# Kernel optimization log

Measured on AMD Instinct MI355X. Metric: run time of the kernel, lower is better.

## Reference

```python
import jax, jax.numpy as jnp
import numpy as np

N_NODES = 100000
LN_EPS = 1e-5
NEG_SLOPE = 0.2


def setup_inputs() -> dict:
    key = jax.random.key(0)
    ks = jax.random.split(key, 6)
    N, E, NIN, EDIM, NOUT, H = N_NODES, 1600000, 64, 32, 128, 4
    x = jax.random.normal(ks[0], (N, NIN), dtype=jnp.float32)
    edge_index = jax.random.randint(ks[1], (2, E), 0, N, dtype=jnp.int64)
    edge_attr = jax.random.normal(ks[2], (E, EDIM), dtype=jnp.float32)
    # xavier-uniform linear weights (torch layout: [out, in])
    def xavier(k, fan_out, fan_in):
        lim = float(np.sqrt(6.0 / (fan_in + fan_out)))
        return jax.random.uniform(k, (fan_out, fan_in), jnp.float32, -lim, lim)
    W_msg = xavier(ks[3], NOUT, NIN + EDIM)          # (128, 96)
    W_att = xavier(ks[4], H, 2 * NIN + EDIM)         # (4, 160)
    bias = jnp.zeros((NOUT,), jnp.float32)
    ln_gamma = jnp.ones((NOUT,), jnp.float32)
    ln_beta = jnp.zeros((NOUT,), jnp.float32)
    return {"x": x, "edge_index": edge_index, "edge_attr": edge_attr,
            "W_msg": W_msg, "W_att": W_att, "bias": bias,
            "ln_gamma": ln_gamma, "ln_beta": ln_beta}


def reference(x, edge_index, edge_attr, W_msg, W_att, bias, ln_gamma, ln_beta):
    N = x.shape[0]
    H = W_att.shape[0]
    src, dst = edge_index[0], edge_index[1]
    xs = x[src]                                       # (E, node_in) gather
    xd = x[dst]                                       # (E, node_in) gather
    # message: W_msg @ [h_u ; x_uv]
    msg_in = jnp.concatenate([xs, edge_attr], axis=-1)            # (E, 96)
    msgs = msg_in @ W_msg.T                                        # (E, out_dim)
    msgs = msgs.reshape(-1, H, W_msg.shape[0] // H)                # (E, H, D)
    # attention logits: LeakyReLU(W_att @ [h_u ; h_v ; x_uv])
    att_in = jnp.concatenate([xs, xd, edge_attr], axis=-1)         # (E, 160)
    logits = att_in @ W_att.T                                      # (E, H)
    logits = jax.nn.leaky_relu(logits, NEG_SLOPE)
    # per-destination-node sparse softmax
    seg_max = jax.ops.segment_max(logits, dst, num_segments=N)     # (N, H)
    exp_l = jnp.exp(logits - seg_max[dst])                         # (E, H)
    seg_sum = jax.ops.segment_sum(exp_l, dst, num_segments=N)      # (N, H)
    att = exp_l / (seg_sum[dst] + 1e-9)                            # (E, H)
    # weighted scatter-add aggregation
    weighted = msgs * att[..., None]                               # (E, H, D)
    out = jax.ops.segment_sum(weighted, dst, num_segments=N)       # (N, H, D)
    out = out.reshape(N, -1) + bias                                # concat heads
    # layer norm over feature dim
    mu = out.mean(axis=-1, keepdims=True)
    var = out.var(axis=-1, keepdims=True)
    out = (out - mu) * jax.lax.rsqrt(var + LN_EPS) * ln_gamma + ln_beta
    return out
```

## Files before the change

### kernel.cpp

```cpp
#include <hip/hip_runtime.h>
#include <hip/hip_bf16.h>

typedef __attribute__((ext_vector_type(8))) short short8;
typedef __attribute__((ext_vector_type(4))) float f32x4;

__device__ __forceinline__ unsigned short fbf(float f) {
  union { float f; unsigned u; } v; v.f = f;
  unsigned r = v.u + 0x7fffu + ((v.u >> 16) & 1u);
  return (unsigned short)(r >> 16);
}
__device__ __forceinline__ unsigned pk2(float a, float b) {
  return (unsigned)fbf(a) | ((unsigned)fbf(b) << 16);
}
__device__ __forceinline__ float ubf(unsigned hi) {
  union { unsigned u; float f; } v; v.u = hi << 16; return v.f;
}
__device__ __forceinline__ float ubf_lo(unsigned u) {
  union { unsigned u; float f; } v; v.u = u << 16; return v.f;
}
__device__ __forceinline__ float ubf_hi(unsigned u) {
  union { unsigned u; float f; } v; v.u = u & 0xffff0000u; return v.f;
}
__device__ __forceinline__ float dot4(float4 a, float4 b) {
  return fmaf(a.x, b.x, fmaf(a.y, b.y, fmaf(a.z, b.z, a.w * b.w)));
}

__launch_bounds__(256)
__global__ void k_phase1(const float* __restrict__ x, const float* __restrict__ W_att,
                         const int* __restrict__ edst, int E,
                         float4* __restrict__ A_s, float4* __restrict__ A_d,
                         unsigned* __restrict__ xb32, int* __restrict__ deg,
                         int* __restrict__ rank, int N) {
  __shared__ float4 s_wa[160];
  if (threadIdx.x < 160) s_wa[threadIdx.x] = ((const float4*)W_att)[threadIdx.x];
  for (int i = blockIdx.x * blockDim.x + threadIdx.x; i < E; i += gridDim.x * blockDim.x)
    rank[i] = atomicAdd(&deg[edst[i]], 1);
  __syncthreads();
  for (int v = blockIdx.x * blockDim.x + threadIdx.x; v < N; v += gridDim.x * blockDim.x) {
    const float4* xp = (const float4*)&x[v * 64];
    float4 xq[16];
    #pragma unroll
    for (int k = 0; k < 16; k++) xq[k] = xp[k];
    float as[4] = {}, ad[4] = {};
    #pragma unroll
    for (int h = 0; h < 4; h++) {
      #pragma unroll
      for (int k = 0; k < 16; k++) {
        as[h] += dot4(s_wa[h * 40 + k], xq[k]);
        ad[h] += dot4(s_wa[h * 40 + 16 + k], xq[k]);
      }
    }
    A_s[v] = make_float4(as[0], as[1], as[2], as[3]);
    A_d[v] = make_float4(ad[0], ad[1], ad[2], ad[3]);
    #pragma unroll
    for (int k = 0; k < 16; k++) {
      xb32[v * 32 + 2 * k]     = pk2(xq[k].x, xq[k].y);
      xb32[v * 32 + 2 * k + 1] = pk2(xq[k].z, xq[k].w);
    }
  }
}

__global__ void k_scan1(const int* __restrict__ deg, int N, int* __restrict__ part,
                        int* __restrict__ bsum) {
  __shared__ int tmp[1024];
  int tid = threadIdx.x;
  int i = blockIdx.x * 1024 + tid;
  int dv = (i < N) ? deg[i] : 0;
  int v = (dv + 7) & ~7;
  tmp[tid] = v;
  __syncthreads();
  for (int ofs = 1; ofs < 1024; ofs <<= 1) {
    int t = (tid >= ofs) ? tmp[tid - ofs] : 0;
    __syncthreads();
    tmp[tid] += t;
    __syncthreads();
  }
  if (i < N) part[i] = tmp[tid] - v;
  if (tid == 1023) bsum[blockIdx.x] = tmp[tid];
}

__global__ void k_scan2(int* __restrict__ part, const int* __restrict__ bsum,
                        const int* __restrict__ deg, int N, int4* __restrict__ csrp) {
  __shared__ int sbase;
  if (threadIdx.x == 0) {
    int b = 0;
    for (int j = 0; j < (int)blockIdx.x; j++) b += bsum[j];
    sbase = b;
  }
  __syncthreads();
  int i = blockIdx.x * 1024 + threadIdx.x;
  if (i < N) {
    const int o = part[i] + sbase;
    part[i] = o;
    const int d = deg[i];
    const int pe = o + ((d + 7) & ~7);
    const int4 z = make_int4(0, 0, 0, 0);
    for (int s = o + d; s < pe; s++) csrp[s] = z;
    if (i == N - 1) part[N] = pe;
  }
}

__launch_bounds__(256)
__global__ void k_fillP(const int* __restrict__ esrc, const int* __restrict__ edst, int E,
                        const float* __restrict__ ea, const float4* __restrict__ A_s,
                        const float4* __restrict__ A_d, const float* __restrict__ W_att,
                        const int* __restrict__ offsets, const int* __restrict__ rank,
                        int4* __restrict__ csrp) {
  __shared__ float4 s_we[32];
  if (threadIdx.x < 32) {
    int h = threadIdx.x >> 3, k4 = threadIdx.x & 7;
    const float* p = &W_att[h * 160 + 128 + k4 * 4];
    s_we[threadIdx.x] = make_float4(p[0], p[1], p[2], p[3]);
  }
  __syncthreads();
  for (int e = blockIdx.x * blockDim.x + threadIdx.x; e < E; e += gridDim.x * blockDim.x) {
    const int s = esrc[e], d = edst[e];
    const int slot = offsets[d] + rank[e];
    const float4* ep = (const float4*)&ea[(unsigned)e * 32u];
    float4 eq[8];
    #pragma unroll
    for (int k = 0; k < 8; k++) eq[k] = ep[k];
    const float4 as4 = A_s[s], ad4 = A_d[d];
    const float base[4] = {as4.x + ad4.x, as4.y + ad4.y, as4.z + ad4.z, as4.w + ad4.w};
    float av[4];
    #pragma unroll
    for (int h = 0; h < 4; h++) {
      float lg = base[h];
      #pragma unroll
      for (int k = 0; k < 8; k++) lg += dot4(s_we[h * 8 + k], eq[k]);
      lg = fmaxf(lg, 0.2f * lg);
      av[h] = __expf(lg);
    }
    csrp[slot] = make_int4(s, e, (int)pk2(av[0], av[1]), (int)pk2(av[2], av[3]));
  }
}

__launch_bounds__(256)
__global__ void k_aggP(const unsigned short* __restrict__ xb, const float* __restrict__ ea,
                       const int4* __restrict__ csrp, const int* __restrict__ offsets,
                       unsigned short* __restrict__ agg, float* __restrict__ denom, int N) {
  __shared__ int4 s_ids[4][32];
  const int lane = threadIdx.x & 63;
  const int wvb = threadIdx.x >> 6;
  const int wv = (blockIdx.x * blockDim.x + threadIdx.x) >> 6;
  const int nw = (gridDim.x * blockDim.x) >> 6;
  const int l32 = lane & 31;
  const bool hi = lane >= 32;

  for (int v0 = wv; v0 < N; v0 += nw) {
    const int vv = __builtin_amdgcn_readfirstlane(v0);
    const int sstart = __builtin_amdgcn_readfirstlane(offsets[vv]);
    const int send = __builtin_amdgcn_readfirstlane(offsets[vv + 1]);
    const int ng = (send - sstart) >> 3;
    const int nq = (ng + 3) >> 2;

    float ax0 = 0, ax1 = 0, ax2 = 0, ax3 = 0;
    float ae0 = 0, ae1 = 0, ae2 = 0, ae3 = 0;
    float dn0 = 0, dn1 = 0, dn2 = 0, dn3 = 0;

    for (int q = 0; q < nq; q++) {
      {
        int4 q_ = csrp[sstart + q * 32 + l32];
        if (lane < 32) s_ids[wvb][l32] = q_;
      }
      const int nsc = min(4, ng - q * 4);
      float ev[4][8];
      unsigned short qv[4][8];
      #pragma unroll
      for (int sc = 0; sc < 4; sc++) {
        if (sc < nsc) {
          #pragma unroll
          for (int p = 0; p < 8; p++) {
            const int4 t_ = s_ids[wvb][sc * 8 + p];
            qv[sc][p] = xb[(unsigned)(t_.x << 6) + lane];
            ev[sc][p] = ea[(unsigned)(t_.y << 5) + l32];
          }
        }
      }
      #pragma unroll
      for (int sc = 0; sc < 4; sc++) {
        if (sc < nsc) {
          #pragma unroll
          for (int p = 0; p < 8; p++) {
            const int4 t_ = s_ids[wvb][sc * 8 + p];
            const float a0_ = ubf_lo((unsigned)t_.z);
            const float a1_ = ubf_hi((unsigned)t_.z);
            const float a2_ = ubf_lo((unsigned)t_.w);
            const float a3_ = ubf_hi((unsigned)t_.w);
            const float xf = ubf((unsigned)qv[sc][p]);
            const float evp = ev[sc][p];
            ax0 = fmaf(a0_, xf, ax0); ax1 = fmaf(a1_, xf, ax1);
            ax2 = fmaf(a2_, xf, ax2); ax3 = fmaf(a3_, xf, ax3);
            ae0 = fmaf(a0_, evp, ae0); ae1 = fmaf(a1_, evp, ae1);
            ae2 = fmaf(a2_, evp, ae2); ae3 = fmaf(a3_, evp, ae3);
            dn0 += a0_; dn1 += a1_; dn2 += a2_; dn3 += a3_;
          }
        }
      }
    }

    const unsigned base = (unsigned)v0 * 384u;
    agg[base + lane]        = fbf(ax0);
    agg[base + 96 + lane]   = fbf(ax1);
    agg[base + 192 + lane]  = fbf(ax2);
    agg[base + 288 + lane]  = fbf(ax3);
    const int hA = hi ? 2 : 0;
    agg[base + hA * 96 + 64 + l32]       = fbf(hi ? ae2 : ae0);
    agg[base + (hA + 1) * 96 + 64 + l32] = fbf(hi ? ae3 : ae1);
    if (lane == 0) ((float4*)denom)[v0] = make_float4(dn0, dn1, dn2, dn3);
  }
}

__launch_bounds__(128)
__global__ void k_out(const unsigned short* __restrict__ agg, const float* __restrict__ W_msg,
                      const float* __restrict__ denom, const float* __restrict__ bias,
                      const float* __restrict__ gamma, const float* __restrict__ beta,
                      float* __restrict__ out, int N, int T) {
  __shared__ float s_den[64];
  __shared__ float s_sum[2][16], s_sq[2][16];
  const int f = threadIdx.x;
  const int w = f >> 6;
  const int l = f & 63;
  const int c16 = l & 15;
  const int rg = l >> 4;

  short8 wb[2][2][3];
  float biasv[2][2], gv[2][2], bv[2][2];
  #pragma unroll
  for (int hh = 0; hh < 2; hh++) {
    const int head = 2 * w + hh;
    #pragma unroll
    for (int ct = 0; ct < 2; ct++) {
      const int q = head * 32 + ct * 16 + c16;
      biasv[hh][ct] = bias[q]; gv[hh][ct] = gamma[q]; bv[hh][ct] = beta[q];
      #pragma unroll
      for (int kk = 0; kk < 3; kk++) {
        const float* p = &W_msg[q * 96 + kk * 32 + rg * 8];
        short8 s;
        #pragma unroll
        for (int i = 0; i < 8; i++) s[i] = (short)fbf(p[i]);
        wb[hh][ct][kk] = s;
      }
    }
  }

  for (int t = blockIdx.x; t < T; t += gridDim.x) {
    const int n0 = t * 16;
    if (f < 64) s_den[f] = denom[min(n0 + (f >> 2), N - 1) * 4 + (f & 3)];
    __syncthreads();

    f32x4 c[2][2] = {{{0.f,0.f,0.f,0.f},{0.f,0.f,0.f,0.f}},
                     {{0.f,0.f,0.f,0.f},{0.f,0.f,0.f,0.f}}};
    const int nA = min(n0 + c16, N - 1);
    #pragma unroll
    for (int hh = 0; hh < 2; hh++) {
      const int head = 2 * w + hh;
      #pragma unroll
      for (int kk = 0; kk < 3; kk++) {
        short8 a = *(const short8*)&agg[nA * 384 + head * 96 + kk * 32 + rg * 8];
        c[hh][0] = __builtin_amdgcn_mfma_f32_16x16x32_bf16(a, wb[hh][0][kk], c[hh][0], 0, 0, 0);
        c[hh][1] = __builtin_amdgcn_mfma_f32_16x16x32_bf16(a, wb[hh][1][kk], c[hh][1], 0, 0, 0);
      }
    }

    float val[2][2][4];
    #pragma unroll
    for (int hh = 0; hh < 2; hh++)
      #pragma unroll
      for (int ct = 0; ct < 2; ct++)
        #pragma unroll
        for (int r = 0; r < 4; r++) {
          const float d = s_den[(rg * 4 + r) * 4 + (2 * w + hh)] + 1e-9f;
          val[hh][ct][r] = c[hh][ct][r] / d + biasv[hh][ct];
        }

    float sr[4], qr[4];
    #pragma unroll
    for (int r = 0; r < 4; r++) {
      float s = 0.f, q2 = 0.f;
      #pragma unroll
      for (int hh = 0; hh < 2; hh++)
        #pragma unroll
        for (int ct = 0; ct < 2; ct++) { s += val[hh][ct][r]; q2 = fmaf(val[hh][ct][r], val[hh][ct][r], q2); }
      #pragma unroll
      for (int m = 1; m <= 8; m <<= 1) { s += __shfl_xor(s, m, 64); q2 += __shfl_xor(q2, m, 64); }
      sr[r] = s; qr[r] = q2;
    }
    if (c16 == 0) {
      #pragma unroll
      for (int r = 0; r < 4; r++) { s_sum[w][rg * 4 + r] = sr[r]; s_sq[w][rg * 4 + r] = qr[r]; }
    }
    __syncthreads();

    float mean[4], rstd[4];
    #pragma unroll
    for (int r = 0; r < 4; r++) {
      const int ni = rg * 4 + r;
      mean[r] = (s_sum[0][ni] + s_sum[1][ni]) * (1.f / 128.f);
      const float m2 = (s_sq[0][ni] + s_sq[1][ni]) * (1.f / 128.f);
      rstd[r] = rsqrtf(m2 - mean[r] * mean[r] + 1e-5f);
    }
    #pragma unroll
    for (int hh = 0; hh < 2; hh++)
      #pragma unroll
      for (int ct = 0; ct < 2; ct++)
        #pragma unroll
        for (int r = 0; r < 4; r++) {
          const int n = n0 + rg * 4 + r;
          if (n < N)
            out[n * 128 + (2 * w + hh) * 32 + ct * 16 + c16] =
                (val[hh][ct][r] - mean[r]) * rstd[r] * gv[hh][ct] + bv[hh][ct];
        }
    __syncthreads();
  }
}

extern "C" void kernel_launch(void* const* d_in, const int* in_sizes, int n_in,
                              void* d_out, int out_size, void* d_ws, size_t ws_size,
                              hipStream_t stream) {
  const float* x     = (const float*)d_in[0];
  const int*   ei    = (const int*)d_in[1];
  const float* ea    = (const float*)d_in[2];
  const float* W_msg = (const float*)d_in[3];
  const float* W_att = (const float*)d_in[4];
  const float* bias  = (const float*)d_in[5];
  const float* gamma = (const float*)d_in[6];
  const float* beta  = (const float*)d_in[7];
  float* out = (float*)d_out;

  const int N = in_sizes[0] / 64;
  const int E = in_sizes[1] / 2;
  const int* esrc = ei;
  const int* edst = ei + E;
  const int EP = E + 8 * N + 64;

  char* p = (char*)d_ws;
  int* deg      = (int*)p;            p += (size_t)N * 4;
  int* offsets  = (int*)p;            p += (size_t)(N + 1) * 4;
  int* rank     = (int*)p;            p += (size_t)E * 4;
  int* bsum     = (int*)p;            p += 2048 * 4;
  int4* csrp    = (int4*)p;           p += (size_t)EP * 16;
  float4* A_s   = (float4*)p;         p += (size_t)N * 16;
  float4* A_d   = (float4*)p;         p += (size_t)N * 16;
  unsigned short* xb = (unsigned short*)p; p += (size_t)N * 64 * 2;
  unsigned short* agg = (unsigned short*)p; p += (size_t)N * 384 * 2;
  float* denom  = (float*)p;

  hipMemsetAsync(deg, 0, (size_t)N * 4, stream);
  const int SB = (N + 1023) / 1024;
  const int T = (N + 15) / 16;

  k_phase1<<<2048, 256, 0, stream>>>(x, W_att, edst, E, A_s, A_d, (unsigned*)xb, deg, rank, N);
  k_scan1<<<SB, 1024, 0, stream>>>(deg, N, offsets, bsum);
  k_scan2<<<SB, 1024, 0, stream>>>(offsets, bsum, deg, N, csrp);
  k_fillP<<<2048, 256, 0, stream>>>(esrc, edst, E, ea, A_s, A_d, W_att, offsets, rank, csrp);
  k_aggP<<<2048, 256, 0, stream>>>(xb, ea, csrp, offsets, agg, denom, N);
  k_out<<<T, 128, 0, stream>>>(agg, W_msg, denom, bias, gamma, beta, out, N, T);
}
```

Baseline: 393.6 us.

## Fuse attention logit computation into aggregation kernel and shrink CSR entries

Moves the per-edge attention logit and exp computation out of the CSR fill kernel and into the per-node aggregation kernel, where edge_attr rows are already being read. The CSR payload shrinks from int4 (src, edge, packed bf16 weights) to int2 (src, edge), and attention weights are now kept in fp32 instead of being rounded to bf16. The aim is to avoid reading edge_attr twice across kernels and to halve CSR write and read traffic. In exchange the aggregation kernel gains shuffles, extra A_s gathers and LDS round-trips per group of 8 edges, and both kernels now launch with a larger grid.

After: 415.4 us. 1.06x slower.

```diff
diff --git a/kernel.cpp b/kernel.cpp
--- a/kernel.cpp
+++ b/kernel.cpp
@@ -14,12 +14,6 @@
 }
 __device__ __forceinline__ float ubf(unsigned hi) {
   union { unsigned u; float f; } v; v.u = hi << 16; return v.f;
-}
-__device__ __forceinline__ float ubf_lo(unsigned u) {
-  union { unsigned u; float f; } v; v.u = u << 16; return v.f;
-}
-__device__ __forceinline__ float ubf_hi(unsigned u) {
-  union { unsigned u; float f; } v; v.u = u & 0xffff0000u; return v.f;
 }
 __device__ __forceinline__ float dot4(float4 a, float4 b) {
   return fmaf(a.x, b.x, fmaf(a.y, b.y, fmaf(a.z, b.z, a.w * b.w)));
@@ -80,7 +74,7 @@
 }
 
 __global__ void k_scan2(int* __restrict__ part, const int* __restrict__ bsum,
-                        const int* __restrict__ deg, int N, int4* __restrict__ csrp) {
+                        const int* __restrict__ deg, int N, int2* __restrict__ csr2) {
   __shared__ int sbase;
   if (threadIdx.x == 0) {
     int b = 0;
@@ -94,63 +88,50 @@
     part[i] = o;
     const int d = deg[i];
     const int pe = o + ((d + 7) & ~7);
-    const int4 z = make_int4(0, 0, 0, 0);
-    for (int s = o + d; s < pe; s++) csrp[s] = z;
+    const int2 z = make_int2(0, 0);
+    for (int s = o + d; s < pe; s++) csr2[s] = z;
     if (i == N - 1) part[N] = pe;
   }
 }
 
 __launch_bounds__(256)
-__global__ void k_fillP(const int* __restrict__ esrc, const int* __restrict__ edst, int E,
-                        const float* __restrict__ ea, const float4* __restrict__ A_s,
-                        const float4* __restrict__ A_d, const float* __restrict__ W_att,
-                        const int* __restrict__ offsets, const int* __restrict__ rank,
-                        int4* __restrict__ csrp) {
-  __shared__ float4 s_we[32];
-  if (threadIdx.x < 32) {
-    int h = threadIdx.x >> 3, k4 = threadIdx.x & 7;
-    const float* p = &W_att[h * 160 + 128 + k4 * 4];
-    s_we[threadIdx.x] = make_float4(p[0], p[1], p[2], p[3]);
-  }
-  __syncthreads();
+__global__ void k_scat2(const int* __restrict__ esrc, const int* __restrict__ edst,
+                        const int* __restrict__ rank, const int* __restrict__ offsets,
+                        int E, int2* __restrict__ csr2) {
   for (int e = blockIdx.x * blockDim.x + threadIdx.x; e < E; e += gridDim.x * blockDim.x) {
-    const int s = esrc[e], d = edst[e];
-    const int slot = offsets[d] + rank[e];
-    const float4* ep = (const float4*)&ea[(unsigned)e * 32u];
-    float4 eq[8];
-    #pragma unroll
-    for (int k = 0; k < 8; k++) eq[k] = ep[k];
-    const float4 as4 = A_s[s], ad4 = A_d[d];
-    const float base[4] = {as4.x + ad4.x, as4.y + ad4.y, as4.z + ad4.z, as4.w + ad4.w};
-    float av[4];
-    #pragma unroll
-    for (int h = 0; h < 4; h++) {
-      float lg = base[h];
-      #pragma unroll
-      for (int k = 0; k < 8; k++) lg += dot4(s_we[h * 8 + k], eq[k]);
-      lg = fmaxf(lg, 0.2f * lg);
-      av[h] = __expf(lg);
-    }
-    csrp[slot] = make_int4(s, e, (int)pk2(av[0], av[1]), (int)pk2(av[2], av[3]));
+    const int d = edst[e];
+    csr2[offsets[d] + rank[e]] = make_int2(esrc[e], e);
   }
 }
 
 __launch_bounds__(256)
-__global__ void k_aggP(const unsigned short* __restrict__ xb, const float* __restrict__ ea,
-                       const int4* __restrict__ csrp, const int* __restrict__ offsets,
+__global__ void k_aggF(const unsigned short* __restrict__ xb, const float* __restrict__ ea,
+                       const float4* __restrict__ A_s, const float4* __restrict__ A_d,
+                       const int2* __restrict__ csr2, const int* __restrict__ offsets,
+                       const int* __restrict__ deg, const float* __restrict__ W_att,
                        unsigned short* __restrict__ agg, float* __restrict__ denom, int N) {
-  __shared__ int4 s_ids[4][32];
+  __shared__ int2 s_ids[4][32];
+  __shared__ float4 s_att[4][8];
   const int lane = threadIdx.x & 63;
   const int wvb = threadIdx.x >> 6;
   const int wv = (blockIdx.x * blockDim.x + threadIdx.x) >> 6;
   const int nw = (gridDim.x * blockDim.x) >> 6;
   const int l32 = lane & 31;
   const bool hi = lane >= 32;
+  const int pj = lane >> 3;
+  const int jc = lane & 7;
+
+  const float4 wea0 = *(const float4*)&W_att[0 * 160 + 128 + jc * 4];
+  const float4 wea1 = *(const float4*)&W_att[1 * 160 + 128 + jc * 4];
+  const float4 wea2 = *(const float4*)&W_att[2 * 160 + 128 + jc * 4];
+  const float4 wea3 = *(const float4*)&W_att[3 * 160 + 128 + jc * 4];
 
   for (int v0 = wv; v0 < N; v0 += nw) {
     const int vv = __builtin_amdgcn_readfirstlane(v0);
     const int sstart = __builtin_amdgcn_readfirstlane(offsets[vv]);
     const int send = __builtin_amdgcn_readfirstlane(offsets[vv + 1]);
+    const int dg = __builtin_amdgcn_readfirstlane(deg[vv]);
+    const float4 adv = A_d[vv];
     const int ng = (send - sstart) >> 3;
     const int nq = (ng + 3) >> 2;
 
@@ -160,7 +141,7 @@
 
     for (int q = 0; q < nq; q++) {
       {
-        int4 q_ = csrp[sstart + q * 32 + l32];
+        int2 q_ = csr2[sstart + q * 32 + l32];
         if (lane < 32) s_ids[wvb][l32] = q_;
       }
       const int nsc = min(4, ng - q * 4);
@@ -171,7 +152,7 @@
         if (sc < nsc) {
           #pragma unroll
           for (int p = 0; p < 8; p++) {
-            const int4 t_ = s_ids[wvb][sc * 8 + p];
+            const int2 t_ = s_ids[wvb][sc * 8 + p];
             qv[sc][p] = xb[(unsigned)(t_.x << 6) + lane];
             ev[sc][p] = ea[(unsigned)(t_.y << 5) + l32];
           }
@@ -180,20 +161,33 @@
       #pragma unroll
       for (int sc = 0; sc < 4; sc++) {
         if (sc < nsc) {
+          const int2 idl = s_ids[wvb][sc * 8 + pj];
+          const float4 ef = *(const float4*)&ea[(unsigned)(idl.y << 5) + jc * 4];
+          const float4 asv = A_s[idl.x];
+          float lp0 = dot4(wea0, ef), lp1 = dot4(wea1, ef);
+          float lp2 = dot4(wea2, ef), lp3 = dot4(wea3, ef);
+          #pragma unroll
+          for (int m = 1; m <= 4; m <<= 1) {
+            lp0 += __shfl_xor(lp0, m, 64); lp1 += __shfl_xor(lp1, m, 64);
+            lp2 += __shfl_xor(lp2, m, 64); lp3 += __shfl_xor(lp3, m, 64);
+          }
+          const float msk = (q * 32 + sc * 8 + pj < dg) ? 1.f : 0.f;
+          float4 av; float lg;
+          lg = lp0 + asv.x + adv.x; lg = fmaxf(lg, 0.2f * lg); av.x = msk * __expf(lg);
+          lg = lp1 + asv.y + adv.y; lg = fmaxf(lg, 0.2f * lg); av.y = msk * __expf(lg);
+          lg = lp2 + asv.z + adv.z; lg = fmaxf(lg, 0.2f * lg); av.z = msk * __expf(lg);
+          lg = lp3 + asv.w + adv.w; lg = fmaxf(lg, 0.2f * lg); av.w = msk * __expf(lg);
+          if (jc == 0) s_att[wvb][pj] = av;
           #pragma unroll
           for (int p = 0; p < 8; p++) {
-            const int4 t_ = s_ids[wvb][sc * 8 + p];
-            const float a0_ = ubf_lo((unsigned)t_.z);
-            const float a1_ = ubf_hi((unsigned)t_.z);
-            const float a2_ = ubf_lo((unsigned)t_.w);
-            const float a3_ = ubf_hi((unsigned)t_.w);
+            const float4 ap = s_att[wvb][p];
             const float xf = ubf((unsigned)qv[sc][p]);
             const float evp = ev[sc][p];
-            ax0 = fmaf(a0_, xf, ax0); ax1 = fmaf(a1_, xf, ax1);
-            ax2 = fmaf(a2_, xf, ax2); ax3 = fmaf(a3_, xf, ax3);
-            ae0 = fmaf(a0_, evp, ae0); ae1 = fmaf(a1_, evp, ae1);
-            ae2 = fmaf(a2_, evp, ae2); ae3 = fmaf(a3_, evp, ae3);
-            dn0 += a0_; dn1 += a1_; dn2 += a2_; dn3 += a3_;
+            ax0 = fmaf(ap.x, xf, ax0); ax1 = fmaf(ap.y, xf, ax1);
+            ax2 = fmaf(ap.z, xf, ax2); ax3 = fmaf(ap.w, xf, ax3);
+            ae0 = fmaf(ap.x, evp, ae0); ae1 = fmaf(ap.y, evp, ae1);
+            ae2 = fmaf(ap.z, evp, ae2); ae3 = fmaf(ap.w, evp, ae3);
+            dn0 += ap.x; dn1 += ap.y; dn2 += ap.z; dn3 += ap.w;
           }
         }
       }
@@ -339,7 +333,7 @@
   int* offsets  = (int*)p;            p += (size_t)(N + 1) * 4;
   int* rank     = (int*)p;            p += (size_t)E * 4;
   int* bsum     = (int*)p;            p += 2048 * 4;
-  int4* csrp    = (int4*)p;           p += (size_t)EP * 16;
+  int2* csr2    = (int2*)p;           p += (size_t)EP * 8;
   float4* A_s   = (float4*)p;         p += (size_t)N * 16;
   float4* A_d   = (float4*)p;         p += (size_t)N * 16;
   unsigned short* xb = (unsigned short*)p; p += (size_t)N * 64 * 2;
@@ -352,8 +346,9 @@
 
   k_phase1<<<2048, 256, 0, stream>>>(x, W_att, edst, E, A_s, A_d, (unsigned*)xb, deg, rank, N);
   k_scan1<<<SB, 1024, 0, stream>>>(deg, N, offsets, bsum);
-  k_scan2<<<SB, 1024, 0, stream>>>(offsets, bsum, deg, N, csrp);
-  k_fillP<<<2048, 256, 0, stream>>>(esrc, edst, E, ea, A_s, A_d, W_att, offsets, rank, csrp);
-  k_aggP<<<2048, 256, 0, stream>>>(xb, ea, csrp, offsets, agg, denom, N);
+  k_scan2<<<SB, 1024, 0, stream>>>(offsets, bsum, deg, N, csr2);
+  k_scat2<<<4096, 256, 0, stream>>>(esrc, edst, rank, offsets, E, csr2);
+  k_aggF<<<4096, 256, 0, stream>>>(xb, ea, A_s, A_d, csr2, offsets, deg, W_att,
+                                   agg, denom, N);
   k_out<<<T, 128, 0, stream>>>(agg, W_msg, denom, bias, gamma, beta, out, N, T);
 }
```
